# Kernel tuning notes

Hardware: AMD Instinct MI355X
Metric: run time of the kernel (lower is better)

Reference implementation:

```python
import jax, jax.numpy as jnp
import numpy as np

IMG_W, IMG_H = 128, 128
N_PTS = 256
MIN_D, MAX_D = 2.0, 6.0
FOCAL = 1.7320508  # 1/tan(fov/2), fov=60deg (FoVPerspectiveCameras default)
SCALING = 0.1      # scaling_factor default
EPS_EA = 1e-10     # pytorch3d EmissionAbsorptionRaymarcher eps


def setup_inputs() -> dict:
    key = jax.random.key(0)
    k1, k2 = jax.random.split(key)
    image3d = jax.random.uniform(k1, (1, 1, 128, 128, 128), jnp.float32)
    opacity = jax.random.uniform(k2, (1, 1, 128, 128, 128), jnp.float32)
    # row-vector camera convention (pytorch3d): p_cam = p_world @ R + T
    R = jnp.zeros((1, 3, 3), jnp.float32).at[:, jnp.arange(3), jnp.arange(3)].set(1.0)
    T = jnp.zeros((1, 3), jnp.float32).at[:, 2].set(4.0)
    return {"image3d": image3d, "opacity": opacity, "R": R, "T": T}


def _trilinear(vol, pts):
    """vol [C,D,H,W]; pts [N,3] xyz in [-1,1] (x->W, y->H, z->D).
    align_corners=True, zero padding outside. Returns [N,C]."""
    C, D, H, W = vol.shape
    x = (pts[:, 0] + 1.0) * 0.5 * (W - 1)
    y = (pts[:, 1] + 1.0) * 0.5 * (H - 1)
    z = (pts[:, 2] + 1.0) * 0.5 * (D - 1)
    x0 = jnp.floor(x); y0 = jnp.floor(y); z0 = jnp.floor(z)
    wx = x - x0; wy = y - y0; wz = z - z0
    vol_flat = vol.reshape(C, -1)
    out = jnp.zeros((pts.shape[0], C), vol.dtype)
    for dz in (0, 1):
        for dy in (0, 1):
            for dx in (0, 1):
                xi = (x0 + dx).astype(jnp.int32)
                yi = (y0 + dy).astype(jnp.int32)
                zi = (z0 + dz).astype(jnp.int32)
                valid = ((xi >= 0) & (xi < W) & (yi >= 0) & (yi < H)
                         & (zi >= 0) & (zi < D))
                w = ((wx if dx else 1.0 - wx) * (wy if dy else 1.0 - wy)
                     * (wz if dz else 1.0 - wz)) * valid.astype(vol.dtype)
                idx = ((jnp.clip(zi, 0, D - 1) * H + jnp.clip(yi, 0, H - 1)) * W
                       + jnp.clip(xi, 0, W - 1))
                vals = jnp.take(vol_flat, idx, axis=1)  # [C,N]
                out = out + w[:, None] * vals.T
    return out


def _forward(image3d, opacity, R, T):
    B = image3d.shape[0]
    features_vol = jnp.repeat(image3d, 3, axis=1)            # [B,3,D,H,W]
    densities_vol = opacity * SCALING                        # [B,1,D,H,W]
    Dv, Hv, Wv = image3d.shape[2:]
    shape = max(image3d.shape[1], image3d.shape[2])
    voxel = 3.0 / shape
    half_extent = voxel * (jnp.array([Wv, Hv, Dv], jnp.float32) - 1.0) / 2.0

    # NDC pixel grid (pytorch3d: +x left, +y up)
    xs = jnp.linspace(1.0, -1.0, IMG_W)
    ys = jnp.linspace(1.0, -1.0, IMG_H)
    gy, gx = jnp.meshgrid(ys, xs, indexing="ij")             # [H,W]
    dirs_cam = jnp.stack([gx / FOCAL, gy / FOCAL, jnp.ones_like(gx)], -1)  # [H,W,3]
    depths = jnp.linspace(MIN_D, MAX_D, N_PTS)               # [P]

    # row-vector transforms: p_world = (p_cam - T) @ R^T
    origins = jnp.einsum("bi,bji->bj", -T, R)                # camera centers [B,3]
    dirs_world = jnp.einsum("hwi,bji->bhwj", dirs_cam, R)    # [B,H,W,3]
    pts = (origins[:, None, None, None, :]
           + depths[None, None, None, :, None] * dirs_world[:, :, :, None, :])
    local = pts / half_extent                                # [B,H,W,P,3]

    pts_flat = local.reshape(B, -1, 3)
    feats = jax.vmap(_trilinear)(features_vol, pts_flat)
    feats = feats.reshape(B, IMG_H, IMG_W, N_PTS, 3)
    dens = jax.vmap(_trilinear)(densities_vol, pts_flat)
    dens = dens.reshape(B, IMG_H, IMG_W, N_PTS)

    # EmissionAbsorption raymarcher
    cum = jnp.cumprod((1.0 + EPS_EA) - dens, axis=-1)
    absorption = jnp.concatenate([jnp.ones_like(cum[..., :1]), cum[..., :-1]], -1)
    weights = dens * absorption
    feat_out = jnp.sum(weights[..., None] * feats, axis=-2)  # [B,H,W,3]
    opac = 1.0 - jnp.prod(1.0 - dens, axis=-1, keepdims=True)
    rgba = jnp.concatenate([feat_out, opac], axis=-1)        # [B,H,W,4]

    screen = jnp.transpose(rgba, (0, 3, 2, 1))               # permute(0,3,2,1)
    gray = screen[:, :3].mean(axis=1, keepdims=True)         # [B,1,W,H]
    st = (gray - gray.mean()) / (gray.std(ddof=1) + 1e-8)    # standardized
    out = (st - st.min() + 1e-8) / (st.max() - st.min() + 1e-8)  # normalized
    return out


def reference(image3d, opacity, R, T):
    return _forward(image3d, opacity, R, T)
```

## Files before the change

kernel.cpp:

```cpp
#include <hip/hip_runtime.h>
#include <math.h>


#define FOCAL 1.7320508f

__global__ __launch_bounds__(1024) void dvr_kernel(
    const float* __restrict__ img, const float* __restrict__ opa,
    const float* __restrict__ Rm, const float* __restrict__ Tv,
    float* __restrict__ g, double* __restrict__ bstats,
    unsigned int* __restrict__ counter, float* __restrict__ out)
{
  const int tid  = threadIdx.x;
  const int lane = tid & 63;
  const int seg  = tid >> 6;
  const int b    = blockIdx.x;
  const int h    = b >> 1;
  const int w    = ((b & 1) << 6) | lane;

  const float R00=Rm[0], R01=Rm[1], R02=Rm[2];
  const float R10=Rm[3], R11=Rm[4], R12=Rm[5];
  const float R20=Rm[6], R21=Rm[7], R22=Rm[8];
  const float T0=Tv[0], T1=Tv[1], T2=Tv[2];

  const float ox = -(T0*R00 + T1*R01 + T2*R02);
  const float oy = -(T0*R10 + T1*R11 + T2*R12);
  const float oz = -(T0*R20 + T1*R21 + T2*R22);

  const float gx = 1.0f - (2.0f/127.0f) * (float)w;
  const float gy = 1.0f - (2.0f/127.0f) * (float)h;
  const float dcx = gx * (1.0f/FOCAL);
  const float dcy = gy * (1.0f/FOCAL);
  const float dwx = dcx*R00 + dcy*R01 + R02;
  const float dwy = dcx*R10 + dcy*R11 + R12;
  const float dwz = dcx*R20 + dcy*R21 + R22;

  const float s_he = (1.0f/1.48828125f) * 63.5f;
  const float ax = dwx * s_he, bxc = ox * s_he + 63.5f;
  const float ay = dwy * s_he, byc = oy * s_he + 63.5f;
  const float az = dwz * s_he, bzc = oz * s_he + 63.5f;

  const int p0 = seg << 4;

  float lp = 1.0f;
  float accl = 0.0f;

  #pragma unroll 4
  for (int j = 0; j < 16; ++j) {
    const float depth = 2.0f + (4.0f/255.0f) * (float)(p0 + j);
    const float x = bxc + depth * ax;
    const float y = byc + depth * ay;
    const float z = bzc + depth * az;
    const float x0f = floorf(x), y0f = floorf(y), z0f = floorf(z);
    const float wx = x - x0f, wy = y - y0f, wz = z - z0f;
    const int x0 = (int)x0f, y0 = (int)y0f, z0 = (int)z0f;

    float feat = 0.0f, dens = 0.0f;
    if (x0 >= -1 && x0 <= 127 && y0 >= -1 && y0 <= 127 &&
        z0 >= -1 && z0 <= 127) {
      const float fx0 = (x0 >= 0)   ? (1.0f - wx) : 0.0f;
      const float fx1 = (x0 <= 126) ? wx          : 0.0f;
      const float fy0 = (y0 >= 0)   ? (1.0f - wy) : 0.0f;
      const float fy1 = (y0 <= 126) ? wy          : 0.0f;
      const float fz0 = (z0 >= 0)   ? (1.0f - wz) : 0.0f;
      const float fz1 = (z0 <= 126) ? wz          : 0.0f;
      const int ix0 = (x0 >= 0)   ? x0     : 0;
      const int ix1 = (x0 <= 126) ? x0 + 1 : 127;
      const int iy0 = ((y0 >= 0)   ? y0     : 0)   << 7;
      const int iy1 = ((y0 <= 126) ? y0 + 1 : 127) << 7;
      const int iz0 = ((z0 >= 0)   ? z0     : 0)   << 14;
      const int iz1 = ((z0 <= 126) ? z0 + 1 : 127) << 14;

      const int b00 = iz0 + iy0, b01 = iz0 + iy1;
      const int b10 = iz1 + iy0, b11 = iz1 + iy1;
      const float w00 = fz0*fy0, w01 = fz0*fy1, w10 = fz1*fy0, w11 = fz1*fy1;

      feat = w00*(fx0*img[b00+ix0] + fx1*img[b00+ix1])
           + w01*(fx0*img[b01+ix0] + fx1*img[b01+ix1])
           + w10*(fx0*img[b10+ix0] + fx1*img[b10+ix1])
           + w11*(fx0*img[b11+ix0] + fx1*img[b11+ix1]);
      dens = w00*(fx0*opa[b00+ix0] + fx1*opa[b00+ix1])
           + w01*(fx0*opa[b01+ix0] + fx1*opa[b01+ix1])
           + w10*(fx0*opa[b10+ix0] + fx1*opa[b10+ix1])
           + w11*(fx0*opa[b11+ix0] + fx1*opa[b11+ix1]);
    }
    const float d = dens * 0.1f;
    accl += feat * d * lp;
    lp   *= (1.0f - d);
  }

  __shared__ float2 slp[16][64];
  slp[seg][lane] = make_float2(accl, lp);
  __syncthreads();

  if (tid < 64) {
    float T = 1.0f, acc = 0.0f;
    #pragma unroll
    for (int s = 0; s < 16; ++s) {
      const float2 v = slp[s][tid];
      acc += v.x * T;
      T *= v.y;
    }
    const int ww = ((b & 1) << 6) | tid;
    g[(ww << 7) + h] = acc;

    double sum = (double)acc;
    double sq  = (double)acc * (double)acc;
    float mn = acc, mx = acc;
    #pragma unroll
    for (int off = 32; off >= 1; off >>= 1) {
      sum += __shfl_xor(sum, off, 64);
      sq  += __shfl_xor(sq,  off, 64);
      mn = fminf(mn, __shfl_xor(mn, off, 64));
      mx = fmaxf(mx, __shfl_xor(mx, off, 64));
    }
    if (tid == 0) {
      bstats[(b << 2) + 0] = sum;
      bstats[(b << 2) + 1] = sq;
      bstats[(b << 2) + 2] = (double)mn;
      bstats[(b << 2) + 3] = (double)mx;
    }
  }
  __syncthreads();

  __shared__ int is_last;
  if (tid == 0) {
    __threadfence();
    const unsigned int old = atomicAdd(counter, 1u);
    is_last = (old == gridDim.x - 1) ? 1 : 0;
  }
  __syncthreads();
  if (!is_last) return;
  __threadfence();

  double S = 0.0, Q = 0.0;
  float MN = 3.402823466e38f, MX = -3.402823466e38f;
  if (tid < 256) {
    S  = bstats[(tid << 2) + 0];
    Q  = bstats[(tid << 2) + 1];
    MN = (float)bstats[(tid << 2) + 2];
    MX = (float)bstats[(tid << 2) + 3];
  }
  #pragma unroll
  for (int off = 32; off >= 1; off >>= 1) {
    S += __shfl_xor(S, off, 64);
    Q += __shfl_xor(Q, off, 64);
    MN = fminf(MN, __shfl_xor(MN, off, 64));
    MX = fmaxf(MX, __shfl_xor(MX, off, 64));
  }
  __shared__ double rs[16], rq[16];
  __shared__ float rmn[16], rmx[16];
  if (lane == 0) { rs[seg] = S; rq[seg] = Q; rmn[seg] = MN; rmx[seg] = MX; }
  __syncthreads();

  __shared__ float cmn, cinvs, csc;
  if (tid == 0) {
    double St = 0.0, Qt = 0.0;
    float MNt = rmn[0], MXt = rmx[0];
    #pragma unroll
    for (int i = 0; i < 4; ++i) {
      St += rs[i]; Qt += rq[i];
      MNt = fminf(MNt, rmn[i]); MXt = fmaxf(MXt, rmx[i]);
    }
    const double mean = St / 16384.0;
    double var = (Qt - 16384.0 * mean * mean) / 16383.0;
    if (var < 0.0) var = 0.0;
    const float sdev = (float)sqrt(var) + 1e-8f;
    cmn   = MNt;
    cinvs = 1.0f / sdev;
    csc   = 1.0f / ((MXt - MNt) / sdev + 1e-8f);
  }
  __syncthreads();

  const float mnv = cmn, invs = cinvs, sc = csc;
  for (int i = tid; i < 16384; i += 1024) {
    out[i] = ((g[i] - mnv) * invs + 1e-8f) * sc;
  }
}

extern "C" void kernel_launch(void* const* d_in, const int* in_sizes, int n_in,
                              void* d_out, int out_size, void* d_ws, size_t ws_size,
                              hipStream_t stream) {
  const float* img = (const float*)d_in[0];
  const float* opa = (const float*)d_in[1];
  const float* Rm  = (const float*)d_in[2];
  const float* Tv  = (const float*)d_in[3];
  float* out = (float*)d_out;

  char* wsb = (char*)d_ws;
  float*        g       = (float*)wsb;
  double*       bstats  = (double*)(wsb + 65536);
  unsigned int* counter = (unsigned int*)(wsb + 65536 + 8192);

  hipMemsetAsync(counter, 0, sizeof(unsigned int), stream);
  dvr_kernel<<<256, 1024, 0, stream>>>(img, opa, Rm, Tv, g, bstats, counter, out);
}
```

Measured before the change: 100.0 us.

## Split each ray's samples across two blocks and combine partials in last block

```diff
diff --git a/kernel.cpp b/kernel.cpp
--- a/kernel.cpp
+++ b/kernel.cpp
@@ -7,15 +7,21 @@
 __global__ __launch_bounds__(1024) void dvr_kernel(
     const float* __restrict__ img, const float* __restrict__ opa,
     const float* __restrict__ Rm, const float* __restrict__ Tv,
-    float* __restrict__ g, double* __restrict__ bstats,
-    unsigned int* __restrict__ counter, float* __restrict__ out)
+    float2* __restrict__ partial, unsigned int* __restrict__ counter,
+    float* __restrict__ out)
 {
+  __shared__ __align__(16) float smem[2080];
+  float2 (*slp)[64]  = (float2(*)[64])smem;
+  float  (*tile)[129] = (float(*)[129])smem;
+
   const int tid  = threadIdx.x;
   const int lane = tid & 63;
   const int seg  = tid >> 6;
-  const int b    = blockIdx.x;
-  const int h    = b >> 1;
-  const int w    = ((b & 1) << 6) | lane;
+  const int blk  = blockIdx.x;
+  const int half = blk & 1;
+  const int pg   = blk >> 1;
+  const int h    = pg >> 1;
+  const int w    = ((pg & 1) << 6) | lane;
 
   const float R00=Rm[0], R01=Rm[1], R02=Rm[2];
   const float R10=Rm[3], R11=Rm[4], R12=Rm[5];
@@ -39,13 +45,13 @@
   const float ay = dwy * s_he, byc = oy * s_he + 63.5f;
   const float az = dwz * s_he, bzc = oz * s_he + 63.5f;
 
-  const int p0 = seg << 4;
+  const int p0 = (((half << 4) | seg) << 3);
 
   float lp = 1.0f;
   float accl = 0.0f;
 
   #pragma unroll 4
-  for (int j = 0; j < 16; ++j) {
+  for (int j = 0; j < 8; ++j) {
     const float depth = 2.0f + (4.0f/255.0f) * (float)(p0 + j);
     const float x = bxc + depth * ax;
     const float y = byc + depth * ay;
@@ -88,7 +94,6 @@
     lp   *= (1.0f - d);
   }
 
-  __shared__ float2 slp[16][64];
   slp[seg][lane] = make_float2(accl, lp);
   __syncthreads();
 
@@ -100,25 +105,8 @@
       acc += v.x * T;
       T *= v.y;
     }
-    const int ww = ((b & 1) << 6) | tid;
-    g[(ww << 7) + h] = acc;
-
-    double sum = (double)acc;
-    double sq  = (double)acc * (double)acc;
-    float mn = acc, mx = acc;
-    #pragma unroll
-    for (int off = 32; off >= 1; off >>= 1) {
-      sum += __shfl_xor(sum, off, 64);
-      sq  += __shfl_xor(sq,  off, 64);
-      mn = fminf(mn, __shfl_xor(mn, off, 64));
-      mx = fmaxf(mx, __shfl_xor(mx, off, 64));
-    }
-    if (tid == 0) {
-      bstats[(b << 2) + 0] = sum;
-      bstats[(b << 2) + 1] = sq;
-      bstats[(b << 2) + 2] = (double)mn;
-      bstats[(b << 2) + 3] = (double)mx;
-    }
+    const int ww = ((pg & 1) << 6) | tid;
+    partial[(half << 14) + (h << 7) + ww] = make_float2(acc, T);
   }
   __syncthreads();
 
@@ -132,13 +120,20 @@
   if (!is_last) return;
   __threadfence();
 
+  float vals[16];
   double S = 0.0, Q = 0.0;
   float MN = 3.402823466e38f, MX = -3.402823466e38f;
-  if (tid < 256) {
-    S  = bstats[(tid << 2) + 0];
-    Q  = bstats[(tid << 2) + 1];
-    MN = (float)bstats[(tid << 2) + 2];
-    MX = (float)bstats[(tid << 2) + 3];
+  #pragma unroll
+  for (int k = 0; k < 16; ++k) {
+    const int pid = (k << 10) + tid;
+    const float2 a  = partial[pid];
+    const float2 b2 = partial[16384 + pid];
+    const float acc = a.x + a.y * b2.x;
+    vals[k] = acc;
+    S += (double)acc;
+    Q += (double)acc * (double)acc;
+    MN = fminf(MN, acc);
+    MX = fmaxf(MX, acc);
   }
   #pragma unroll
   for (int off = 32; off >= 1; off >>= 1) {
@@ -152,12 +147,12 @@
   if (lane == 0) { rs[seg] = S; rq[seg] = Q; rmn[seg] = MN; rmx[seg] = MX; }
   __syncthreads();
 
-  __shared__ float cmn, cinvs, csc;
+  __shared__ float cs[3];
   if (tid == 0) {
     double St = 0.0, Qt = 0.0;
     float MNt = rmn[0], MXt = rmx[0];
     #pragma unroll
-    for (int i = 0; i < 4; ++i) {
+    for (int i = 0; i < 16; ++i) {
       St += rs[i]; Qt += rq[i];
       MNt = fminf(MNt, rmn[i]); MXt = fmaxf(MXt, rmx[i]);
     }
@@ -165,15 +160,26 @@
     double var = (Qt - 16384.0 * mean * mean) / 16383.0;
     if (var < 0.0) var = 0.0;
     const float sdev = (float)sqrt(var) + 1e-8f;
-    cmn   = MNt;
-    cinvs = 1.0f / sdev;
-    csc   = 1.0f / ((MXt - MNt) / sdev + 1e-8f);
-  }
-  __syncthreads();
-
-  const float mnv = cmn, invs = cinvs, sc = csc;
-  for (int i = tid; i < 16384; i += 1024) {
-    out[i] = ((g[i] - mnv) * invs + 1e-8f) * sc;
+    cs[0] = MNt;
+    cs[1] = 1.0f / sdev;
+    cs[2] = 1.0f / ((MXt - MNt) / sdev + 1e-8f);
+  }
+  __syncthreads();
+  const float mnv = cs[0], invs = cs[1], sc = cs[2];
+
+  const int hi = tid >> 7;
+  const int wc = tid & 127;
+  const int r  = tid & 15;
+  const int w0 = tid >> 4;
+  #pragma unroll
+  for (int c = 0; c < 8; ++c) {
+    __syncthreads();
+    tile[hi][wc]     = vals[2*c];
+    tile[8 + hi][wc] = vals[2*c + 1];
+    __syncthreads();
+    const int hh = (c << 4) + r;
+    out[(w0      << 7) + hh] = ((tile[r][w0]      - mnv) * invs + 1e-8f) * sc;
+    out[((w0+64) << 7) + hh] = ((tile[r][w0 + 64] - mnv) * invs + 1e-8f) * sc;
   }
 }
 
@@ -187,10 +193,9 @@
   float* out = (float*)d_out;
 
   char* wsb = (char*)d_ws;
-  float*        g       = (float*)wsb;
-  double*       bstats  = (double*)(wsb + 65536);
-  unsigned int* counter = (unsigned int*)(wsb + 65536 + 8192);
+  float2*       partial = (float2*)wsb;
+  unsigned int* counter = (unsigned int*)(wsb + 262144);
 
   hipMemsetAsync(counter, 0, sizeof(unsigned int), stream);
-  dvr_kernel<<<256, 1024, 0, stream>>>(img, opa, Rm, Tv, g, bstats, counter, out);
+  dvr_kernel<<<512, 1024, 0, stream>>>(img, opa, Rm, Tv, partial, counter, out);
 }
```

After: 107.8 us. 1.08x slower.
